# Kernel optimization log

Measured on AMD Instinct MI355X. Metric: run time of the kernel, lower is better.

## Reference

```python
import jax, jax.numpy as jnp
import numpy as np
import math

E = 1024      # embed_dim
H = 16        # num_heads
D = 32        # head_dim = E // H // 2
DEPTH = 12
LAMBDA_INIT = 0.8 - 0.6 * math.exp(-0.3 * DEPTH)
B, T = 4, 1024
EPS = 1e-5


def setup_inputs() -> dict:
    key = jax.random.key(0)
    ks = jax.random.split(key, 10)
    s = 0.02  # realistic init scale for weight matrices
    return {
        "x": jax.random.normal(ks[0], (B, T, E), jnp.float32),
        "Wq": jax.random.normal(ks[1], (E, E), jnp.float32) * s,
        "Wk": jax.random.normal(ks[2], (E, E), jnp.float32) * s,
        "Wv": jax.random.normal(ks[3], (E, E), jnp.float32) * s,
        "Wo": jax.random.normal(ks[4], (E, E), jnp.float32) * s,
        "lambda_q1": jax.random.normal(ks[5], (D,), jnp.float32) * 0.1,
        "lambda_k1": jax.random.normal(ks[6], (D,), jnp.float32) * 0.1,
        "lambda_q2": jax.random.normal(ks[7], (D,), jnp.float32) * 0.1,
        "lambda_k2": jax.random.normal(ks[8], (D,), jnp.float32) * 0.1,
        "g": jnp.ones((2 * D,), jnp.float32),  # subln affine weight
    }


def reference(x, Wq, Wk, Wv, Wo, lambda_q1, lambda_k1, lambda_q2, lambda_k2, g):
    b, t, _ = x.shape
    scaling = D ** -0.5
    # projections (torch Linear: x @ W.T), split into 2H half-width q/k heads
    q = (x @ Wq.T).reshape(b, t, 2 * H, D).transpose(0, 2, 1, 3) * scaling  # [b,2H,t,D]
    k = (x @ Wk.T).reshape(b, t, 2 * H, D).transpose(0, 2, 1, 3)            # [b,2H,t,D]
    v = (x @ Wv.T).reshape(b, t, H, 2 * D).transpose(0, 2, 1, 3)            # [b,H,t,2D]
    # dual score maps, fp32 softmax
    aw = jnp.einsum('bhqd,bhkd->bhqk', q, k)               # [b,2H,t,t]
    aw = jnp.nan_to_num(aw)
    aw = jax.nn.softmax(aw.astype(jnp.float32), axis=-1).astype(q.dtype)
    # scalar lambda
    lam1 = jnp.exp(jnp.sum(lambda_q1 * lambda_k1))
    lam2 = jnp.exp(jnp.sum(lambda_q2 * lambda_k2))
    lam = lam1 - lam2 + LAMBDA_INIT
    # differential subtract of the paired softmax maps
    aw = aw.reshape(b, H, 2, t, t)
    aw = aw[:, :, 0] - lam * aw[:, :, 1]                   # [b,H,t,t]
    attn = jnp.einsum('bhqk,bhkd->bhqd', aw, v)            # [b,H,t,2D]
    # per-head RMSNorm over 2D channel dim (affine)
    attn = attn * jax.lax.rsqrt(jnp.mean(attn * attn, axis=-1, keepdims=True) + EPS) * g
    attn = attn * (1.0 - LAMBDA_INIT)
    attn = attn.transpose(0, 2, 1, 3).reshape(b, t, H * 2 * D)  # [b,t,E]
    return attn @ Wo.T
```

## Files before the change

kernel.cpp:

```cpp
#include <hip/hip_runtime.h>
#include <math.h>

#define E_   1024
#define H_   16
#define B_   4
#define T_   1024
#define LAMBDA_INIT 0.783605766532f
#define SCALE_Q 0.17677669529663687f

typedef short s16x8 __attribute__((ext_vector_type(8)));
typedef float f32x4 __attribute__((ext_vector_type(4)));

#define SWZ(c, r) ((((c) ^ ((r) & 7)) * 8))

__device__ inline ushort f2bf(float x) {
    unsigned u = __builtin_bit_cast(unsigned, x);
    u += 0x7fffu + ((u >> 16) & 1u);
    return (ushort)(u >> 16);
}

__device__ inline uint f2bf2(float lo, float hi) {
#if __has_builtin(__builtin_amdgcn_cvt_pk_bf16_f32)
    typedef __bf16 bf16x2_t __attribute__((ext_vector_type(2)));
    bf16x2_t r = __builtin_amdgcn_cvt_pk_bf16_f32(lo, hi);
    return __builtin_bit_cast(uint, r);
#else
    uint ul = __builtin_bit_cast(uint, lo);
    uint uh = __builtin_bit_cast(uint, hi);
    ul += 0x7fffu + ((ul >> 16) & 1u);
    uh += 0x7fffu + ((uh >> 16) & 1u);
    return __builtin_amdgcn_perm(uh, ul, 0x07060302u);
#endif
}

__device__ inline void gl_lds16(const ushort* g, ushort* l) {
    __builtin_amdgcn_global_load_lds((const __attribute__((address_space(1))) void*)g,
                                     (__attribute__((address_space(3))) void*)l,
                                     16, 0, 0);
}

__global__ __launch_bounds__(256) void prep(
    const float* __restrict__ x,  const float* __restrict__ Wq,
    const float* __restrict__ Wk, const float* __restrict__ Wv,
    const float* __restrict__ Wo,
    const float* __restrict__ lq1, const float* __restrict__ lk1,
    const float* __restrict__ lq2, const float* __restrict__ lk2,
    ushort* __restrict__ xb, ushort* __restrict__ Wqb, ushort* __restrict__ Wkb,
    ushort* __restrict__ Wvb, ushort* __restrict__ Wob, float* __restrict__ lamp)
{
    const int blk = blockIdx.x;
    const int tid = threadIdx.x;
    if (blk >= 4096) {
        if (tid < 64) {
            float p1 = 0.f, p2 = 0.f;
            if (tid < 32) { p1 = lq1[tid] * lk1[tid]; p2 = lq2[tid] * lk2[tid]; }
            #pragma unroll
            for (int off = 32; off; off >>= 1) {
                p1 += __shfl_xor(p1, off);
                p2 += __shfl_xor(p2, off);
            }
            if (tid == 0) lamp[0] = expf(p1) - expf(p2) + LAMBDA_INIT;
        }
        return;
    }
    const float* in;
    ushort* out;
    int base;
    if (blk < 2048) { in = x; out = xb; base = blk; }
    else {
        int t = blk - 2048, w = t >> 9;
        base = t & 511;
        in  = w == 0 ? Wq  : (w == 1 ? Wk  : (w == 2 ? Wv  : Wo));
        out = w == 0 ? Wqb : (w == 1 ? Wkb : (w == 2 ? Wvb : Wob));
    }
    int i = (base * 256 + tid) * 8;
    float4 a = *(const float4*)&in[i];
    float4 b = *(const float4*)&in[i + 4];
    union { ushort u[8]; uint4 v; } o;
    o.u[0] = f2bf(a.x); o.u[1] = f2bf(a.y); o.u[2] = f2bf(a.z); o.u[3] = f2bf(a.w);
    o.u[4] = f2bf(b.x); o.u[5] = f2bf(b.y); o.u[6] = f2bf(b.z); o.u[7] = f2bf(b.w);
    *(uint4*)&out[i] = o.v;
}

__global__ __launch_bounds__(256) void gemm_qkv(
    const ushort* __restrict__ Xb, const ushort* __restrict__ Wqb,
    const ushort* __restrict__ Wkb, const ushort* __restrict__ Wvb,
    ushort* __restrict__ QK, ushort* __restrict__ Vt)
{
    __shared__ ushort As[128 * 32];
    __shared__ ushort Ws[128 * 32];
    const int tid = threadIdx.x;
    const int wave = tid >> 6, lane = tid & 63;
    const int l15 = lane & 15, quad = lane >> 4;
    const int bm = blockIdx.y * 128;
    const int bng = blockIdx.x * 128;
    const int region = bng >> 10;
    const ushort* W = region == 0 ? Wqb : (region == 1 ? Wkb : Wvb);
    const float scale = region == 0 ? SCALE_Q : 1.0f;
    const int wn = bng & 1023;
    const int lrow = lane >> 2;
    const int lcol = (lane & 3) * 8;

    f32x4 acc[4][4] = {};
    const int wr = wave >> 1, wc = wave & 1;

    for (int k0 = 0; k0 < 1024; k0 += 32) {
        #pragma unroll
        for (int p = 0; p < 2; ++p) {
            int i = wave + 4 * p;
            gl_lds16(&Xb[(size_t)(bm + i * 16 + lrow) * 1024 + k0 + lcol], &As[i * 512]);
            gl_lds16(&W [(size_t)(wn + i * 16 + lrow) * 1024 + k0 + lcol], &Ws[i * 512]);
        }
        __syncthreads();
        s16x8 a[4], b[4];
        #pragma unroll
        for (int i = 0; i < 4; ++i)
            a[i] = *(const s16x8*)&As[(wr * 64 + i * 16 + l15) * 32 + quad * 8];
        #pragma unroll
        for (int j = 0; j < 4; ++j)
            b[j] = *(const s16x8*)&Ws[(wc * 64 + j * 16 + l15) * 32 + quad * 8];
        #pragma unroll
        for (int i = 0; i < 4; ++i)
            #pragma unroll
            for (int j = 0; j < 4; ++j)
                acc[i][j] = __builtin_amdgcn_mfma_f32_16x16x32_bf16(a[i], b[j], acc[i][j], 0, 0, 0);
        __syncthreads();
    }

    if (region < 2) {
        #pragma unroll
        for (int i = 0; i < 4; ++i)
            #pragma unroll
            for (int j = 0; j < 4; ++j)
                #pragma unroll
                for (int r = 0; r < 4; ++r) {
                    int row = bm + wr * 64 + i * 16 + quad * 4 + r;
                    int col = region * 1024 + wn + wc * 64 + j * 16 + l15;
                    QK[(size_t)row * 2048 + col] = f2bf(acc[i][j][r] * scale);
                }
    } else {
        const int bb = bm >> 10;
        const int t0 = (bm & 1023) + wr * 64 + quad * 4;
        #pragma unroll
        for (int i = 0; i < 4; ++i)
            #pragma unroll
            for (int j = 0; j < 4; ++j) {
                int e = wn + wc * 64 + j * 16 + l15;
                ushort4 o;
                o.x = f2bf(acc[i][j][0]); o.y = f2bf(acc[i][j][1]);
                o.z = f2bf(acc[i][j][2]); o.w = f2bf(acc[i][j][3]);
                *(ushort4*)&Vt[((size_t)bb * E_ + e) * T_ + t0 + i * 16] = o;
            }
    }
}

__global__ __launch_bounds__(256) void gemm_out(
    const ushort* __restrict__ Ab, const ushort* __restrict__ Wob,
    float* __restrict__ C)
{
    __shared__ ushort As[64 * 32];
    __shared__ ushort Ws[128 * 32];
    const int tid = threadIdx.x;
    const int wave = tid >> 6, lane = tid & 63;
    const int l15 = lane & 15, quad = lane >> 4;
    const int bm = blockIdx.y * 64;
    const int bn = blockIdx.x * 128;
    const int lrow = lane >> 2;
    const int lcol = (lane & 3) * 8;

    f32x4 acc[2][4] = {};
    const int wr = wave >> 1, wc = wave & 1;

    for (int k0 = 0; k0 < 1024; k0 += 32) {
        gl_lds16(&Ab[(size_t)(bm + wave * 16 + lrow) * 1024 + k0 + lcol], &As[wave * 512]);
        #pragma unroll
        for (int p = 0; p < 2; ++p) {
            int i = wave + 4 * p;
            gl_lds16(&Wob[(size_t)(bn + i * 16 + lrow) * 1024 + k0 + lcol], &Ws[i * 512]);
        }
        __syncthreads();
        s16x8 a[2], b[4];
        #pragma unroll
        for (int i = 0; i < 2; ++i)
            a[i] = *(const s16x8*)&As[(wr * 32 + i * 16 + l15) * 32 + quad * 8];
        #pragma unroll
        for (int j = 0; j < 4; ++j)
            b[j] = *(const s16x8*)&Ws[(wc * 64 + j * 16 + l15) * 32 + quad * 8];
        #pragma unroll
        for (int i = 0; i < 2; ++i)
            #pragma unroll
            for (int j = 0; j < 4; ++j)
                acc[i][j] = __builtin_amdgcn_mfma_f32_16x16x32_bf16(a[i], b[j], acc[i][j], 0, 0, 0);
        __syncthreads();
    }

    #pragma unroll
    for (int i = 0; i < 2; ++i)
        #pragma unroll
        for (int j = 0; j < 4; ++j)
            #pragma unroll
            for (int r = 0; r < 4; ++r) {
                int row = bm + wr * 32 + i * 16 + quad * 4 + r;
                int col = bn + wc * 64 + j * 16 + l15;
                C[(size_t)row * 1024 + col] = acc[i][j][r];
            }
}

__global__ __launch_bounds__(256, 4) void diff_attn(
    const ushort* __restrict__ QK, const ushort* __restrict__ Vt,
    const float* __restrict__ g, const float* __restrict__ lamp,
    ushort* __restrict__ O)
{
    __shared__ __align__(16) ushort Ks[2][4096];
    __shared__ __align__(16) ushort Vts[2][4096];
    __shared__ __align__(16) ushort Pt[4][1024];

    const int tid  = threadIdx.x;
    const int lane = tid & 63;
    const int wave = tid >> 6;
    const int l15  = lane & 15;
    const int quad = lane >> 4;

    const int blk = blockIdx.x;
    const int bh = blk & 63;
    const int qt = blk >> 6;
    const int b  = bh >> 4;
    const int h  = bh & 15;
    const int q0 = qt * 64;
    const int hoff = h * 64;
    const size_t rowbase = (size_t)b * T_;

    const ushort* Qg = QK;
    const ushort* Kg = QK + 1024;
    const size_t vtbase = ((size_t)b * E_ + hoff) * T_;

    const int lr  = lane >> 3;
    const int jsw = ((lane & 7) ^ lr) * 8;

    const size_t qrow = (rowbase + q0 + wave * 16 + l15) * 2048 + hoff;
    s16x8 aq0 = *(const s16x8*)&Qg[qrow + quad * 8];
    s16x8 aq1 = *(const s16x8*)&Qg[qrow + 32 + quad * 8];

    const int kaoff0 = l15 * 64 + SWZ(quad,     l15);
    const int kaoff1 = l15 * 64 + SWZ(4 + quad, l15);
    const int pfoff0 = l15 * 64 + SWZ(quad,     l15);
    const int pfoff1 = l15 * 64 + SWZ(4 + quad, l15);
    ushort* myPt = &Pt[wave][0];

    const f32x4 zf = {0.f, 0.f, 0.f, 0.f};
    f32x4 o0[4] = {zf, zf, zf, zf};
    f32x4 o1[4] = {zf, zf, zf, zf};
    float lsum0 = 0.f, lsum1 = 0.f;

    {
        #pragma unroll
        for (int p = 0; p < 2; ++p) {
            int r = wave * 16 + p * 8;
            gl_lds16(&Kg[(rowbase + r + lr) * 2048 + hoff + jsw], &Ks[0][r * 64]);
            gl_lds16(&Vt[vtbase + (size_t)(r + lr) * T_ + jsw],   &Vts[0][r * 64]);
        }
    }
    __syncthreads();

    for (int kt = 0; kt < 16; ++kt) {
        const int cur = kt & 1;
        const int nxt = cur ^ 1;
        {
            const int ktn = (kt + 1) & 15;
            #pragma unroll
            for (int p = 0; p < 2; ++p) {
                int r = wave * 16 + p * 8;
                gl_lds16(&Kg[(rowbase + ktn * 64 + r + lr) * 2048 + hoff + jsw],
                         &Ks[nxt][r * 64]);
                gl_lds16(&Vt[vtbase + (size_t)(r + lr) * T_ + ktn * 64 + jsw],
                         &Vts[nxt][r * 64]);
            }
        }

        s16x8 va[4][2];
        #pragma unroll
        for (int jt = 0; jt < 4; ++jt) {
            va[jt][0] = *(const s16x8*)&Vts[cur][jt * 1024 + pfoff0];
            va[jt][1] = *(const s16x8*)&Vts[cur][jt * 1024 + pfoff1];
        }

        {
            f32x4 S[4];
            #pragma unroll
            for (int jk = 0; jk < 4; ++jk) {
                s16x8 ka = *(const s16x8*)&Ks[cur][jk * 1024 + kaoff0];
                S[jk] = __builtin_amdgcn_mfma_f32_16x16x32_bf16(ka, aq0, zf, 0, 0, 0);
            }
            #pragma unroll
            for (int jk = 0; jk < 4; ++jk) {
                float e0 = __expf(S[jk][0]), e1 = __expf(S[jk][1]);
                float e2 = __expf(S[jk][2]), e3 = __expf(S[jk][3]);
                lsum0 += (e0 + e1) + (e2 + e3);
                uint2 pk; pk.x = f2bf2(e0, e1); pk.y = f2bf2(e2, e3);
                *(uint2*)&myPt[l15 * 64 + SWZ(2 * jk + (quad >> 1), l15) + (quad & 1) * 4] = pk;
            }
            #pragma unroll
            for (int h2 = 0; h2 < 2; ++h2) {
                s16x8 pf = *(const s16x8*)&myPt[h2 ? pfoff1 : pfoff0];
                #pragma unroll
                for (int jt = 0; jt < 4; ++jt)
                    o0[jt] = __builtin_amdgcn_mfma_f32_16x16x32_bf16(va[jt][h2], pf, o0[jt], 0, 0, 0);
            }
        }
        {
            f32x4 S[4];
            #pragma unroll
            for (int jk = 0; jk < 4; ++jk) {
                s16x8 ka = *(const s16x8*)&Ks[cur][jk * 1024 + 32 + kaoff1 - SWZ(4 + quad, l15) + SWZ(4 + quad, l15)];
                ka = *(const s16x8*)&Ks[cur][jk * 1024 + kaoff1];
                S[jk] = __builtin_amdgcn_mfma_f32_16x16x32_bf16(ka, aq1, zf, 0, 0, 0);
            }
            #pragma unroll
            for (int jk = 0; jk < 4; ++jk) {
                float e0 = __expf(S[jk][0]), e1 = __expf(S[jk][1]);
                float e2 = __expf(S[jk][2]), e3 = __expf(S[jk][3]);
                lsum1 += (e0 + e1) + (e2 + e3);
                uint2 pk; pk.x = f2bf2(e0, e1); pk.y = f2bf2(e2, e3);
                *(uint2*)&myPt[l15 * 64 + SWZ(2 * jk + (quad >> 1), l15) + (quad & 1) * 4] = pk;
            }
            #pragma unroll
            for (int h2 = 0; h2 < 2; ++h2) {
                s16x8 pf = *(const s16x8*)&myPt[h2 ? pfoff1 : pfoff0];
                #pragma unroll
                for (int jt = 0; jt < 4; ++jt)
                    o1[jt] = __builtin_amdgcn_mfma_f32_16x16x32_bf16(va[jt][h2], pf, o1[jt], 0, 0, 0);
            }
        }
        __syncthreads();
    }

    lsum0 += __shfl_xor(lsum0, 16); lsum0 += __shfl_xor(lsum0, 32);
    lsum1 += __shfl_xor(lsum1, 16); lsum1 += __shfl_xor(lsum1, 32);

    const float lam = lamp[0];
    const float fin = 1.f - LAMBDA_INIT;
    float i0 = 1.f / lsum0;
    float i1 = lam / lsum1;
    float val[4][4];
    float ssq = 0.f;
    #pragma unroll
    for (int jt = 0; jt < 4; ++jt)
        #pragma unroll
        for (int r = 0; r < 4; ++r) {
            float v = o0[jt][r] * i0 - o1[jt][r] * i1;
            val[jt][r] = v;
            ssq += v * v;
        }
    ssq += __shfl_xor(ssq, 16);
    ssq += __shfl_xor(ssq, 32);
    float sc = rsqrtf(ssq * (1.f / 64.f) + 1e-5f) * fin;
    size_t rowoff = (rowbase + q0 + wave * 16 + l15) * 1024 + hoff;
    #pragma unroll
    for (int jt = 0; jt < 4; ++jt) {
        float4 gv = *(const float4*)&g[jt * 16 + quad * 4];
        uint p01 = f2bf2(val[jt][0] * sc * gv.x, val[jt][1] * sc * gv.y);
        uint p23 = f2bf2(val[jt][2] * sc * gv.z, val[jt][3] * sc * gv.w);
        *(uint*)&O[rowoff + jt * 16 + quad * 4 + 0] = p01;
        *(uint*)&O[rowoff + jt * 16 + quad * 4 + 2] = p23;
    }
}

extern "C" void kernel_launch(void* const* d_in, const int* in_sizes, int n_in,
                              void* d_out, int out_size, void* d_ws, size_t ws_size,
                              hipStream_t stream)
{
    const float* x   = (const float*)d_in[0];
    const float* Wq  = (const float*)d_in[1];
    const float* Wk  = (const float*)d_in[2];
    const float* Wv  = (const float*)d_in[3];
    const float* Wo  = (const float*)d_in[4];
    const float* lq1 = (const float*)d_in[5];
    const float* lk1 = (const float*)d_in[6];
    const float* lq2 = (const float*)d_in[7];
    const float* lk2 = (const float*)d_in[8];
    const float* g   = (const float*)d_in[9];
    float* out = (float*)d_out;

    const int M = B_ * T_;
    const size_t ME = (size_t)M * E_;
    const size_t EE = (size_t)E_ * E_;
    ushort* xb  = (ushort*)d_ws;
    ushort* Wqb = xb  + ME;
    ushort* Wkb = Wqb + EE;
    ushort* Wvb = Wkb + EE;
    ushort* Wob = Wvb + EE;
    ushort* QK  = Wob + EE;
    ushort* Vtb = QK + (size_t)M * 2048;
    float*  lamp = (float*)(Vtb + ME);
    ushort* Ab  = xb;

    prep<<<4097, 256, 0, stream>>>(x, Wq, Wk, Wv, Wo, lq1, lk1, lq2, lk2,
                                   xb, Wqb, Wkb, Wvb, Wob, lamp);
    gemm_qkv<<<dim3(24, 32), 256, 0, stream>>>(xb, Wqb, Wkb, Wvb, QK, Vtb);
    diff_attn<<<B_ * H_ * (T_ / 64), 256, 0, stream>>>(QK, Vtb, g, lamp, Ab);
    gemm_out<<<dim3(8, 64), 256, 0, stream>>>(Ab, Wob, out);
}
```

Baseline: 206.6 us.

## Double-buffer LDS in projection GEMMs and vectorize epilogue stores via swapped MFMA operands

Both the QKV and output GEMMs now use two LDS buffers, issuing the next k-tile's global-to-LDS loads before computing on the current tile, with one barrier per iteration instead of two. The MFMA operand order is swapped for the Q/K and output paths so each lane holds four consecutive columns, letting the epilogue write ushort4/float4 instead of scalar strided stores. The attention kernel gets only cleanup of duplicate offset variables and a dead load. LDS use in the GEMMs doubles, which may reduce occupancy.

```diff
diff --git a/kernel.cpp b/kernel.cpp
--- a/kernel.cpp
+++ b/kernel.cpp
@@ -87,8 +87,8 @@
     const ushort* __restrict__ Wkb, const ushort* __restrict__ Wvb,
     ushort* __restrict__ QK, ushort* __restrict__ Vt)
 {
-    __shared__ ushort As[128 * 32];
-    __shared__ ushort Ws[128 * 32];
+    __shared__ ushort As[2][128 * 32];
+    __shared__ ushort Ws[2][128 * 32];
     const int tid = threadIdx.x;
     const int wave = tid >> 6, lane = tid & 63;
     const int l15 = lane & 15, quad = lane >> 4;
@@ -104,40 +104,60 @@
     f32x4 acc[4][4] = {};
     const int wr = wave >> 1, wc = wave & 1;
 
+    #pragma unroll
+    for (int p = 0; p < 2; ++p) {
+        int i = wave + 4 * p;
+        gl_lds16(&Xb[(size_t)(bm + i * 16 + lrow) * 1024 + lcol], &As[0][i * 512]);
+        gl_lds16(&W [(size_t)(wn + i * 16 + lrow) * 1024 + lcol], &Ws[0][i * 512]);
+    }
+    __syncthreads();
+
     for (int k0 = 0; k0 < 1024; k0 += 32) {
-        #pragma unroll
-        for (int p = 0; p < 2; ++p) {
-            int i = wave + 4 * p;
-            gl_lds16(&Xb[(size_t)(bm + i * 16 + lrow) * 1024 + k0 + lcol], &As[i * 512]);
-            gl_lds16(&W [(size_t)(wn + i * 16 + lrow) * 1024 + k0 + lcol], &Ws[i * 512]);
+        const int cur = (k0 >> 5) & 1, nxt = cur ^ 1;
+        if (k0 + 32 < 1024) {
+            #pragma unroll
+            for (int p = 0; p < 2; ++p) {
+                int i = wave + 4 * p;
+                gl_lds16(&Xb[(size_t)(bm + i * 16 + lrow) * 1024 + k0 + 32 + lcol], &As[nxt][i * 512]);
+                gl_lds16(&W [(size_t)(wn + i * 16 + lrow) * 1024 + k0 + 32 + lcol], &Ws[nxt][i * 512]);
+            }
+        }
+        s16x8 a[4], b[4];
+        #pragma unroll
+        for (int i = 0; i < 4; ++i)
+            a[i] = *(const s16x8*)&As[cur][(wr * 64 + i * 16 + l15) * 32 + quad * 8];
+        #pragma unroll
+        for (int j = 0; j < 4; ++j)
+            b[j] = *(const s16x8*)&Ws[cur][(wc * 64 + j * 16 + l15) * 32 + quad * 8];
+        if (region < 2) {
+            #pragma unroll
+            for (int i = 0; i < 4; ++i)
+                #pragma unroll
+                for (int j = 0; j < 4; ++j)
+                    acc[i][j] = __builtin_amdgcn_mfma_f32_16x16x32_bf16(b[j], a[i], acc[i][j], 0, 0, 0);
+        } else {
+            #pragma unroll
+            for (int i = 0; i < 4; ++i)
+                #pragma unroll
+                for (int j = 0; j < 4; ++j)
+                    acc[i][j] = __builtin_amdgcn_mfma_f32_16x16x32_bf16(a[i], b[j], acc[i][j], 0, 0, 0);
         }
         __syncthreads();
-        s16x8 a[4], b[4];
-        #pragma unroll
-        for (int i = 0; i < 4; ++i)
-            a[i] = *(const s16x8*)&As[(wr * 64 + i * 16 + l15) * 32 + quad * 8];
-        #pragma unroll
-        for (int j = 0; j < 4; ++j)
-            b[j] = *(const s16x8*)&Ws[(wc * 64 + j * 16 + l15) * 32 + quad * 8];
-        #pragma unroll
-        for (int i = 0; i < 4; ++i)
-            #pragma unroll
-            for (int j = 0; j < 4; ++j)
-                acc[i][j] = __builtin_amdgcn_mfma_f32_16x16x32_bf16(a[i], b[j], acc[i][j], 0, 0, 0);
-        __syncthreads();
     }
 
     if (region < 2) {
         #pragma unroll
-        for (int i = 0; i < 4; ++i)
-            #pragma unroll
-            for (int j = 0; j < 4; ++j)
-                #pragma unroll
-                for (int r = 0; r < 4; ++r) {
-                    int row = bm + wr * 64 + i * 16 + quad * 4 + r;
-                    int col = region * 1024 + wn + wc * 64 + j * 16 + l15;
-                    QK[(size_t)row * 2048 + col] = f2bf(acc[i][j][r] * scale);
-                }
+        for (int i = 0; i < 4; ++i) {
+            int row = bm + wr * 64 + i * 16 + l15;
+            #pragma unroll
+            for (int j = 0; j < 4; ++j) {
+                int col = region * 1024 + wn + wc * 64 + j * 16 + quad * 4;
+                ushort4 o;
+                o.x = f2bf(acc[i][j][0] * scale); o.y = f2bf(acc[i][j][1] * scale);
+                o.z = f2bf(acc[i][j][2] * scale); o.w = f2bf(acc[i][j][3] * scale);
+                *(ushort4*)&QK[(size_t)row * 2048 + col] = o;
+            }
+        }
     } else {
         const int bb = bm >> 10;
         const int t0 = (bm & 1023) + wr * 64 + quad * 4;
@@ -158,8 +178,8 @@
     const ushort* __restrict__ Ab, const ushort* __restrict__ Wob,
     float* __restrict__ C)
 {
-    __shared__ ushort As[64 * 32];
-    __shared__ ushort Ws[128 * 32];
+    __shared__ ushort As[2][64 * 32];
+    __shared__ ushort Ws[2][128 * 32];
     const int tid = threadIdx.x;
     const int wave = tid >> 6, lane = tid & 63;
     const int l15 = lane & 15, quad = lane >> 4;
@@ -171,39 +191,51 @@
     f32x4 acc[2][4] = {};
     const int wr = wave >> 1, wc = wave & 1;
 
+    gl_lds16(&Ab[(size_t)(bm + wave * 16 + lrow) * 1024 + lcol], &As[0][wave * 512]);
+    #pragma unroll
+    for (int p = 0; p < 2; ++p) {
+        int i = wave + 4 * p;
+        gl_lds16(&Wob[(size_t)(bn + i * 16 + lrow) * 1024 + lcol], &Ws[0][i * 512]);
+    }
+    __syncthreads();
+
     for (int k0 = 0; k0 < 1024; k0 += 32) {
-        gl_lds16(&Ab[(size_t)(bm + wave * 16 + lrow) * 1024 + k0 + lcol], &As[wave * 512]);
-        #pragma unroll
-        for (int p = 0; p < 2; ++p) {
-            int i = wave + 4 * p;
-            gl_lds16(&Wob[(size_t)(bn + i * 16 + lrow) * 1024 + k0 + lcol], &Ws[i * 512]);
-        }
+        const int cur = (k0 >> 5) & 1, nxt = cur ^ 1;
+        if (k0 + 32 < 1024) {
+            gl_lds16(&Ab[(size_t)(bm + wave * 16 + lrow) * 1024 + k0 + 32 + lcol], &As[nxt][wave * 512]);
+            #pragma unroll
+            for (int p = 0; p < 2; ++p) {
+                int i = wave + 4 * p;
+                gl_lds16(&Wob[(size_t)(bn + i * 16 + lrow) * 1024 + k0 + 32 + lcol], &Ws[nxt][i * 512]);
+            }
+        }
+        s16x8 a[2], b[4];
+        #pragma unroll
+        for (int i = 0; i < 2; ++i)
+            a[i] = *(const s16x8*)&As[cur][(wr * 32 + i * 16 + l15) * 32 + quad * 8];
+        #pragma unroll
+        for (int j = 0; j < 4; ++j)
+            b[j] = *(const s16x8*)&Ws[cur][(wc * 64 + j * 16 + l15) * 32 + quad * 8];
+        #pragma unroll
+        for (int i = 0; i < 2; ++i)
+            #pragma unroll
+            for (int j = 0; j < 4; ++j)
+                acc[i][j] = __builtin_amdgcn_mfma_f32_16x16x32_bf16(b[j], a[i], acc[i][j], 0, 0, 0);
         __syncthreads();
-        s16x8 a[2], b[4];
-        #pragma unroll
-        for (int i = 0; i < 2; ++i)
-            a[i] = *(const s16x8*)&As[(wr * 32 + i * 16 + l15) * 32 + quad * 8];
-        #pragma unroll
-        for (int j = 0; j < 4; ++j)
-            b[j] = *(const s16x8*)&Ws[(wc * 64 + j * 16 + l15) * 32 + quad * 8];
-        #pragma unroll
-        for (int i = 0; i < 2; ++i)
-            #pragma unroll
-            for (int j = 0; j < 4; ++j)
-                acc[i][j] = __builtin_amdgcn_mfma_f32_16x16x32_bf16(a[i], b[j], acc[i][j], 0, 0, 0);
-        __syncthreads();
-    }
-
-    #pragma unroll
-    for (int i = 0; i < 2; ++i)
-        #pragma unroll
-        for (int j = 0; j < 4; ++j)
-            #pragma unroll
-            for (int r = 0; r < 4; ++r) {
-                int row = bm + wr * 32 + i * 16 + quad * 4 + r;
-                int col = bn + wc * 64 + j * 16 + l15;
-                C[(size_t)row * 1024 + col] = acc[i][j][r];
-            }
+    }
+
+    #pragma unroll
+    for (int i = 0; i < 2; ++i) {
+        int row = bm + wr * 32 + i * 16 + l15;
+        #pragma unroll
+        for (int j = 0; j < 4; ++j) {
+            int col = bn + wc * 64 + j * 16 + quad * 4;
+            float4 o;
+            o.x = acc[i][j][0]; o.y = acc[i][j][1];
+            o.z = acc[i][j][2]; o.w = acc[i][j][3];
+            *(float4*)&C[(size_t)row * 1024 + col] = o;
+        }
+    }
 }
 
 __global__ __launch_bounds__(256, 4) void diff_attn(
@@ -243,8 +275,6 @@
 
     const int kaoff0 = l15 * 64 + SWZ(quad,     l15);
     const int kaoff1 = l15 * 64 + SWZ(4 + quad, l15);
-    const int pfoff0 = l15 * 64 + SWZ(quad,     l15);
-    const int pfoff1 = l15 * 64 + SWZ(4 + quad, l15);
     ushort* myPt = &Pt[wave][0];
 
     const f32x4 zf = {0.f, 0.f, 0.f, 0.f};
@@ -252,13 +282,11 @@
     f32x4 o1[4] = {zf, zf, zf, zf};
     float lsum0 = 0.f, lsum1 = 0.f;
 
-    {
-        #pragma unroll
-        for (int p = 0; p < 2; ++p) {
-            int r = wave * 16 + p * 8;
-            gl_lds16(&Kg[(rowbase + r + lr) * 2048 + hoff + jsw], &Ks[0][r * 64]);
-            gl_lds16(&Vt[vtbase + (size_t)(r + lr) * T_ + jsw],   &Vts[0][r * 64]);
-        }
+    #pragma unroll
+    for (int p = 0; p < 2; ++p) {
+        int r = wave * 16 + p * 8;
+        gl_lds16(&Kg[(rowbase + r + lr) * 2048 + hoff + jsw], &Ks[0][r * 64]);
+        gl_lds16(&Vt[vtbase + (size_t)(r + lr) * T_ + jsw],   &Vts[0][r * 64]);
     }
     __syncthreads();
 
@@ -280,8 +308,8 @@
         s16x8 va[4][2];
         #pragma unroll
         for (int jt = 0; jt < 4; ++jt) {
-            va[jt][0] = *(const s16x8*)&Vts[cur][jt * 1024 + pfoff0];
-            va[jt][1] = *(const s16x8*)&Vts[cur][jt * 1024 + pfoff1];
+            va[jt][0] = *(const s16x8*)&Vts[cur][jt * 1024 + kaoff0];
+            va[jt][1] = *(const s16x8*)&Vts[cur][jt * 1024 + kaoff1];
         }
 
         {
@@ -301,7 +329,7 @@
             }
             #pragma unroll
             for (int h2 = 0; h2 < 2; ++h2) {
-                s16x8 pf = *(const s16x8*)&myPt[h2 ? pfoff1 : pfoff0];
+                s16x8 pf = *(const s16x8*)&myPt[h2 ? kaoff1 : kaoff0];
                 #pragma unroll
                 for (int jt = 0; jt < 4; ++jt)
                     o0[jt] = __builtin_amdgcn_mfma_f32_16x16x32_bf16(va[jt][h2], pf, o0[jt], 0, 0, 0);
@@ -311,8 +339,7 @@
             f32x4 S[4];
             #pragma unroll
             for (int jk = 0; jk < 4; ++jk) {
-                s16x8 ka = *(const s16x8*)&Ks[cur][jk * 1024 + 32 + kaoff1 - SWZ(4 + quad, l15) + SWZ(4 + quad, l15)];
-                ka = *(const s16x8*)&Ks[cur][jk * 1024 + kaoff1];
+                s16x8 ka = *(const s16x8*)&Ks[cur][jk * 1024 + kaoff1];
                 S[jk] = __builtin_amdgcn_mfma_f32_16x16x32_bf16(ka, aq1, zf, 0, 0, 0);
             }
             #pragma unroll
@@ -325,7 +352,7 @@
             }
             #pragma unroll
             for (int h2 = 0; h2 < 2; ++h2) {
-                s16x8 pf = *(const s16x8*)&myPt[h2 ? pfoff1 : pfoff0];
+                s16x8 pf = *(const s16x8*)&myPt[h2 ? kaoff1 : kaoff0];
                 #pragma unroll
                 for (int jt = 0; jt < 4; ++jt)
                     o1[jt] = __builtin_amdgcn_mfma_f32_16x16x32_bf16(va[jt][h2], pf, o1[jt], 0, 0, 0);
```

Result: slower. 220.5 us (+6.7%).
